# Kernel optimization log

Hardware: AMD Instinct MI355X
Metric: run time of the kernel (lower is better)

## Reference

```python
import jax, jax.numpy as jnp
import numpy as np
from jax.scipy.special import digamma

T, K, D = 8192, 64, 128


def setup_inputs() -> dict:
    key = jax.random.key(0)
    ks = jax.random.split(key, 7)
    mu_t = jax.random.normal(ks[0], (T, D), jnp.float32)
    diag_var_t = jax.random.uniform(ks[1], (T, D), jnp.float32)  # encoder diag variances >= 0
    niw_mu = jax.random.normal(ks[2], (K, D), jnp.float32)
    A = jax.random.normal(ks[3], (K, D, D), jnp.float32) / np.sqrt(D)
    niw_Psi = jnp.einsum('kde,kfe->kdf', A, A) + float(D) * jnp.eye(D, dtype=jnp.float32)[None]  # SPD
    niw_nu = D + 2.0 + 10.0 * jax.random.uniform(ks[4], (K,), jnp.float32)  # nu > D+1
    phi = 0.1 + 4.0 * jax.random.uniform(ks[5], (K, K), jnp.float32)  # Dirichlet posterior params > 0
    log_pi = jax.nn.log_softmax(jax.random.normal(ks[6], (K,), jnp.float32))
    return dict(mu_t=mu_t, diag_var_t=diag_var_t, niw_mu=niw_mu, niw_Psi=niw_Psi,
                niw_nu=niw_nu, phi=phi, log_pi=log_pi)


def _emission_logB(mu_t, diag_var_t, niw_mu, niw_Psi, niw_nu):
    # E[Lambda_k] = nu_k * Psi_k^{-1}; E[log|Lambda_k|] via multivariate digamma
    L = jnp.linalg.cholesky(niw_Psi)                                  # [K,D,D]
    logdet_Psi = 2.0 * jnp.sum(jnp.log(jnp.diagonal(L, axis1=-2, axis2=-1)), axis=-1)  # [K]
    eye = jnp.broadcast_to(jnp.eye(D, dtype=niw_Psi.dtype), (K, D, D))
    Psi_inv = jax.scipy.linalg.cho_solve((L, True), eye)              # [K,D,D]
    E_Lam = niw_nu[:, None, None] * Psi_inv                           # [K,D,D]
    i = jnp.arange(1, D + 1, dtype=niw_Psi.dtype)[None, :]            # [1,D]
    E_logdet = jnp.sum(digamma((niw_nu[:, None] + 1.0 - i) / 2.0), axis=1) \
        + D * jnp.log(jnp.asarray(2.0, niw_Psi.dtype)) - logdet_Psi   # [K]
    diagv = jnp.clip(diag_var_t, 0.0)                                 # [T,D]
    diff = mu_t[:, None, :] - niw_mu[None, :, :]                      # [T,K,D]
    quad_mean = jnp.einsum('tkd,kde,tke->tk', diff, E_Lam, diff)      # [T,K]
    ELam_diag = jnp.diagonal(E_Lam, axis1=-2, axis2=-1)               # [K,D]
    trace_diag = jnp.einsum('td,kd->tk', diagv, ELam_diag)            # [T,K]
    const = -0.5 * D * jnp.log(jnp.asarray(2.0 * np.pi, mu_t.dtype))
    return 0.5 * E_logdet[None, :] + const - 0.5 * (quad_mean + trace_diag)


def _forward_backward(log_pi, ElogA, logB):
    a0 = log_pi + logB[0]
    z0 = jax.nn.logsumexp(a0)
    alpha0 = a0 - z0

    def fwd_step(aprev, logb):
        pred = jax.nn.logsumexp(aprev[:, None] + ElogA, axis=0)
        a = pred + logb
        z = jax.nn.logsumexp(a)
        return a - z, (a - z, z)

    _, (alpha_rest, z_rest) = jax.lax.scan(fwd_step, alpha0, logB[1:])
    alpha = jnp.concatenate([alpha0[None], alpha_rest], axis=0)       # [T,K]
    logZ = jnp.concatenate([z0[None], z_rest], axis=0)                # [T]

    def bwd_step(bnext, xs):
        logb_next, z_next = xs
        b = jax.nn.logsumexp(ElogA + (logb_next + bnext)[None, :], axis=1) - z_next
        return b, b

    beta_T = jnp.zeros_like(alpha0)
    _, beta_rest = jax.lax.scan(bwd_step, beta_T, (logB[1:], logZ[1:]), reverse=True)
    beta = jnp.concatenate([beta_rest, beta_T[None]], axis=0)         # [T,K]

    rhat_log = alpha + beta
    rhat_log = rhat_log - jax.nn.logsumexp(rhat_log, axis=1, keepdims=True)
    rhat = jnp.exp(rhat_log)

    x = alpha[:-1, :, None] + ElogA[None, :, :] + (logB[1:] + beta[1:])[:, None, :]  # [T-1,K,K]
    x = x - jax.nn.logsumexp(x.reshape(x.shape[0], -1), axis=1)[:, None, None]
    xihat = jnp.exp(x)

    ll = jnp.sum(logZ)
    return rhat, xihat, ll


def reference(mu_t, diag_var_t, niw_mu, niw_Psi, niw_nu, phi, log_pi):
    logB = _emission_logB(mu_t, diag_var_t, niw_mu, niw_Psi, niw_nu)  # [T,K]
    ElogA = digamma(phi) - digamma(jnp.sum(phi, axis=1, keepdims=True))  # [K,K]
    rhat, xihat, ll = _forward_backward(log_pi, ElogA, logB)
    return rhat, xihat, ll
```

## Files before the change

### kernel.cpp

```cpp
#include <hip/hip_runtime.h>
#include <math.h>

#define T_LEN 8192
#define KK 64
#define DD 128
#define RS 132
#define GP 68

typedef __bf16  bf16x4 __attribute__((ext_vector_type(4)));
typedef __bf16  bf16x8 __attribute__((ext_vector_type(8)));
typedef float  f32x16 __attribute__((ext_vector_type(16)));

__device__ __forceinline__ float wred_max(float v){
#pragma unroll
  for (int m = 1; m < 64; m <<= 1) v = fmaxf(v, __shfl_xor(v, m, 64));
  return v;
}
__device__ __forceinline__ float wred_sum(float v){
#pragma unroll
  for (int m = 1; m < 64; m <<= 1) v += __shfl_xor(v, m, 64);
  return v;
}
__device__ __forceinline__ float digamma_f(float x){
  float r = 0.f;
  while (x < 6.f){ r -= 1.f/x; x += 1.f; }
  float ix = 1.f/x, ix2 = ix*ix;
  return r + logf(x) - 0.5f*ix - ix2*(0.0833333333f - ix2*(0.0083333333f - ix2*0.0039682540f));
}

__global__ void __launch_bounds__(256, 1) k_neumann(
    const float* __restrict__ Psi, const float* __restrict__ niw_mu,
    const float* __restrict__ nu_, const float* __restrict__ phi,
    __bf16* __restrict__ Ebf, float* __restrict__ EdiagT,
    float* __restrict__ cvecT, float* __restrict__ rK, float* __restrict__ Lhalf,
    float* __restrict__ sclK,
    float* __restrict__ ElogA, float* __restrict__ P, float* __restrict__ PT)
{
  extern __shared__ float lds[];
  float* Rl = lds;
  float* Pb = lds + DD*RS;
  __shared__ float red[256];
  __shared__ float msh[DD];
  int k = blockIdx.x, tid = threadIdx.x;
  const float* A = Psi + (size_t)k*DD*DD;

  if (tid < 64){
    float ph = phi[k*KK + tid];
    float s  = wred_sum(ph);
    float e  = digamma_f(ph) - digamma_f(s);
    ElogA[k*KK + tid] = e;
    float p = expf(e);
    P [k*KK + tid] = p;
    PT[tid*KK + k] = p;
  }

  float tl = 0.f;
  for (int d = tid; d < DD; d += 256) tl += A[d*DD + d];
  red[tid] = tl; __syncthreads();
  for (int off = 128; off > 0; off >>= 1){ if (tid < off) red[tid] += red[tid+off]; __syncthreads(); }
  float c = red[0] / (float)DD;
  __syncthreads();

  float trpow = 0.f;
  for (int idx = tid; idx < DD*DD; idx += 256){
    int d = idx >> 7, e = idx & 127;
    float v = ((d == e) ? 1.f : 0.f) - A[idx]/c;
    Rl[d*RS + e] = v;
    if (d == e) trpow += v;
  }
  __syncthreads();

  int tr = tid >> 4, tc = tid & 15;
  int r0 = tr*8, c0 = tc*8;
  float S[8][8];
#pragma unroll
  for (int i = 0; i < 8; i++)
#pragma unroll
// ... 62 lines not shown
#pragma unroll
  for (int i = 0; i < 8; i++)
#pragma unroll
    for (int j = 0; j < 8; j++){
      float sv = S[i][j];
      bool dg = (r0+i == c0+j);
      if (dg) EdiagT[(r0+i)*KK + k] = scl*sv;
      float et = scl*(sv - (dg ? 1.f : 0.f));
      int r = (r0+i)*DD + (c0+j);
      Ebf[(size_t)(r>>4)*1024 + k*16 + (r&15)] = (__bf16)et;
    }
#pragma unroll
  for (int i = 0; i < 8; i++){
    float4 w0, w1;
    w0.x=S[i][0]; w0.y=S[i][1]; w0.z=S[i][2]; w0.w=S[i][3];
    w1.x=S[i][4]; w1.y=S[i][5]; w1.z=S[i][6]; w1.w=S[i][7];
    *(float4*)&Pb[(r0+i)*RS + c0]     = w0;
    *(float4*)&Pb[(r0+i)*RS + c0 + 4] = w1;
  }
  for (int d = tid; d < DD; d += 256) msh[d] = niw_mu[k*DD + d];
  __syncthreads();
  float cv = 0.f;
  if (tid < DD){
    float acc = 0.f;
    for (int e = 0; e < DD; e++) acc += Pb[tid*RS + e]*msh[e];
    cv = scl*acc;
    cvecT[tid*KK + k] = cv;
  }
  red[tid] = (tid < DD) ? msh[tid]*cv : 0.f; __syncthreads();
  for (int off = 128; off > 0; off >>= 1){ if (tid < off) red[tid] += red[tid+off]; __syncthreads(); }
  if (tid == 0) rK[k] = red[0];
}

__global__ void __launch_bounds__(256, 1) k_q1(const float* __restrict__ mu,
      const __bf16* __restrict__ Ebf, float* __restrict__ part)
{
  __shared__ float muF[32*132];
  __shared__ float trb[128*66];
  int b = blockIdx.x;
  int rs = b & 3, tseg = b >> 2;
  int t0 = tseg*128, d0 = rs*32;
  int tid = threadIdx.x;
  int w = tid >> 6, lane = tid & 63;
  int kh = w & 1, th = w >> 1;
  int l31 = lane & 31;
  int k0 = (lane >> 5)*8;

  for (int v = tid; v < 128*32; v += 256){
    int t = v >> 5, d = v & 31;
    muF[d*132 + t] = mu[(size_t)(t0+t)*DD + d0 + d];
  }

  bf16x8 Bf0[8], Bf1[8];
#pragma unroll
  for (int c = 0; c < 8; c++){
    int tc0 = t0 + th*64 + l31;
    int tc1 = tc0 + 32;
    float4 x0 = *(const float4*)&mu[(size_t)tc0*DD + c*16 + k0];
    float4 x1 = *(const float4*)&mu[(size_t)tc0*DD + c*16 + k0 + 4];
    bf16x8 hv;
    hv[0]=(__bf16)x0.x; hv[1]=(__bf16)x0.y; hv[2]=(__bf16)x0.z; hv[3]=(__bf16)x0.w;
    hv[4]=(__bf16)x1.x; hv[5]=(__bf16)x1.y; hv[6]=(__bf16)x1.z; hv[7]=(__bf16)x1.w;
    Bf0[c] = hv;
    float4 y0 = *(const float4*)&mu[(size_t)tc1*DD + c*16 + k0];
    float4 y1 = *(const float4*)&mu[(size_t)tc1*DD + c*16 + k0 + 4];
    bf16x8 gv;
    gv[0]=(__bf16)y0.x; gv[1]=(__bf16)y0.y; gv[2]=(__bf16)y0.z; gv[3]=(__bf16)y0.w;
    gv[4]=(__bf16)y1.x; gv[5]=(__bf16)y1.y; gv[6]=(__bf16)y1.z; gv[7]=(__bf16)y1.w;
    Bf1[c] = gv;
  }
  __syncthreads();

  const unsigned short* __restrict__ Eu = (const unsigned short*)Ebf;
  size_t abase = (size_t)(kh*32 + l31)*16 + k0;

  f32x16 acc0, acc1;
#pragma unroll
  for (int i = 0; i < 16; i++){ acc0[i]=0.f; acc1[i]=0.f; }

  uint4 A0[8], A1[8];
  {
    const unsigned short* ap = Eu + (size_t)d0*8192 + abase;
#pragma unroll
    for (int c = 0; c < 8; c++) A0[c] = *(const uint4*)(ap + c*1024);
#pragma unroll
    for (int c = 0; c < 8; c++) A1[c] = *(const uint4*)(ap + 8192 + c*1024);
  }

  for (int dd = 0; dd < 32; dd += 2){
    {
      f32x16 ta, tb;
#pragma unroll
      for (int i = 0; i < 16; i++){ ta[i]=0.f; tb[i]=0.f; }
#pragma unroll
      for (int c = 0; c < 8; c++){
        bf16x8 av = *(bf16x8*)&A0[c];
        ta = __builtin_amdgcn_mfma_f32_32x32x16_bf16(av, Bf0[c], ta, 0, 0, 0);
        tb = __builtin_amdgcn_mfma_f32_32x32x16_bf16(av, Bf1[c], tb, 0, 0, 0);
      }
      float m0 = muF[dd*132 + th*64 + l31];
      float m1 = muF[dd*132 + th*64 + 32 + l31];
#pragma unroll
      for (int i = 0; i < 16; i++){
        acc0[i] = fmaf(m0, ta[i], acc0[i]);
        acc1[i] = fmaf(m1, tb[i], acc1[i]);
      }
    }
    if (dd + 2 < 32){
      const unsigned short* ap = Eu + (size_t)(d0+dd+2)*8192 + abase;
#pragma unroll
      for (int c = 0; c < 8; c++) A0[c] = *(const uint4*)(ap + c*1024);
    }
    {
      f32x16 ta, tb;
#pragma unroll
      for (int i = 0; i < 16; i++){ ta[i]=0.f; tb[i]=0.f; }
#pragma unroll
      for (int c = 0; c < 8; c++){
        bf16x8 av = *(bf16x8*)&A1[c];
        ta = __builtin_amdgcn_mfma_f32_32x32x16_bf16(av, Bf0[c], ta, 0, 0, 0);
        tb = __builtin_amdgcn_mfma_f32_32x32x16_bf16(av, Bf1[c], tb, 0, 0, 0);
      }
      float m0 = muF[(dd+1)*132 + th*64 + l31];
      float m1 = muF[(dd+1)*132 + th*64 + 32 + l31];
#pragma unroll
      for (int i = 0; i < 16; i++){
        acc0[i] = fmaf(m0, ta[i], acc0[i]);
        acc1[i] = fmaf(m1, tb[i], acc1[i]);
      }
    }
    if (dd + 3 < 32){
      const unsigned short* ap = Eu + (size_t)(d0+dd+3)*8192 + abase;
#pragma unroll
      for (int c = 0; c < 8; c++) A1[c] = *(const uint4*)(ap + c*1024);
    }
  }

  __syncthreads();
#pragma unroll
  for (int r = 0; r < 16; r++){
    int krow = kh*32 + (r&3) + 8*(r>>2) + 4*(lane>>5);
    trb[(th*64 + l31)*66 + krow]      = acc0[r];
    trb[(th*64 + 32 + l31)*66 + krow] = acc1[r];
  }
  __syncthreads();
  float* dst = part + (size_t)rs*T_LEN*KK;
  {
    int t = tid >> 1, kc = (tid & 1)*32;
#pragma unroll
    for (int q = 0; q < 8; q++){
      float4 vv = *(float4*)&trb[t*66 + kc + q*4];
      *(float4*)&dst[(size_t)(t0+t)*KK + kc + q*4] = vv;
    }
  }
}

__global__ void __launch_bounds__(256) k_logBall(
    const float* __restrict__ part, const float* __restrict__ mu, const float* __restrict__ dvar,
    const float* __restrict__ cvecT, const float* __restrict__ EdiagT,
    const float* __restrict__ rK, const float* __restrict__ Lhalf, const float* __restrict__ sclK,
    float* __restrict__ logB, float* __restrict__ mrow, float* __restrict__ btil)
{
  int tid = threadIdx.x; int k = tid & 63; int w = tid >> 6;
  float rk = rK[k], lh = Lhalf[k], scl = sclK[k];
  int tbase = blockIdx.x*32 + w*8;
  float a1[8], a2[8], ssv[8];
#pragma unroll
  for (int tt = 0; tt < 8; tt++){ a1[tt]=0.f; a2[tt]=0.f; ssv[tt]=0.f; }
  for (int dc = 0; dc < DD; dc += 4){
    float c0 = cvecT[(dc+0)*KK + k], c1 = cvecT[(dc+1)*KK + k];
    float c2 = cvecT[(dc+2)*KK + k], c3 = cvecT[(dc+3)*KK + k];
    float e0 = EdiagT[(dc+0)*KK + k], e1 = EdiagT[(dc+1)*KK + k];
    float e2 = EdiagT[(dc+2)*KK + k], e3 = EdiagT[(dc+3)*KK + k];
#pragma unroll
    for (int tt = 0; tt < 8; tt++){
      float4 m4 = *(const float4*)(mu   + (size_t)(tbase+tt)*DD + dc);
      float4 v4 = *(const float4*)(dvar + (size_t)(tbase+tt)*DD + dc);
      a1[tt] = fmaf(m4.x,c0, fmaf(m4.y,c1, fmaf(m4.z,c2, fmaf(m4.w,c3, a1[tt]))));
      a2[tt] = fmaf(fmaxf(v4.x,0.f),e0, fmaf(fmaxf(v4.y,0.f),e1,
               fmaf(fmaxf(v4.z,0.f),e2, fmaf(fmaxf(v4.w,0.f),e3, a2[tt]))));
      ssv[tt] = fmaf(m4.x,m4.x, fmaf(m4.y,m4.y, fmaf(m4.z,m4.z, fmaf(m4.w,m4.w, ssv[tt]))));
    }
  }
#pragma unroll
  for (int tt = 0; tt < 8; tt++){
    int t = tbase + tt;
    float q = scl*ssv[tt]
            + part[(size_t)0*T_LEN*KK + (size_t)t*KK + k]
            + part[(size_t)1*T_LEN*KK + (size_t)t*KK + k]
            + part[(size_t)2*T_LEN*KK + (size_t)t*KK + k]
            + part[(size_t)3*T_LEN*KK + (size_t)t*KK + k];
    float lb = lh - 0.5f*(q - 2.f*a1[tt] + rk + a2[tt]);
    float m  = wred_max(lb);
    logB[(size_t)t*KK + k] = lb;
    btil[(size_t)t*KK + k] = expf(lb - m);
    if (k == 0) mrow[t] = m;
  }
}

__global__ void __launch_bounds__(128, 1) k_pass1(const float* __restrict__ Pm,
     const float* __restrict__ btil, float* __restrict__ G8)
{
  __shared__ float G[64*GP];
  __shared__ float wmax[2][2];
  int tid = threadIdx.x, w = tid >> 6, lane = tid & 63;
  int chunk = blockIdx.x;
  int kb8 = (lane >> 5)*8;
  int n = lane & 31;

  bf16x8 Bhi[4][2], Blo[4][2];
#pragma unroll
  for (int Kb = 0; Kb < 4; Kb++)
#pragma unroll
    for (int J = 0; J < 2; J++){
#pragma unroll
      for (int j = 0; j < 8; j++){
        float p = Pm[(Kb*16 + kb8 + j)*KK + J*32 + n];
        __bf16 h = (__bf16)p;
        Bhi[Kb][J][j] = h;
        Blo[Kb][J][j] = (__bf16)(p - (float)h);
      }
    }
  for (int v = tid; v < 64*64; v += 128){
    int i = v >> 6, j = v & 63;
    G[i*GP + j] = (i == j) ? 1.f : 0.f;
  }
  __syncthreads();

  int m = w*32 + n;
// ... 81 lines not shown
      float4 x0 = *(const float4*)&X[m*GP + Kb*16 + kb8];
      float4 x1 = *(const float4*)&X[m*GP + Kb*16 + kb8 + 4];
      float xv[8] = {x0.x,x0.y,x0.z,x0.w,x1.x,x1.y,x1.z,x1.w};
      bf16x8 ah, al;
#pragma unroll
      for (int q = 0; q < 8; q++){
        __bf16 h = (__bf16)xv[q];
        ah[q] = h;
        al[q] = (__bf16)(xv[q] - (float)h);
      }
      acc0 = __builtin_amdgcn_mfma_f32_32x32x16_bf16(ah, Bh[Kb][0], acc0, 0,0,0);
      acc0 = __builtin_amdgcn_mfma_f32_32x32x16_bf16(ah, Bl[Kb][0], acc0, 0,0,0);
      acc0 = __builtin_amdgcn_mfma_f32_32x32x16_bf16(al, Bh[Kb][0], acc0, 0,0,0);
      acc1 = __builtin_amdgcn_mfma_f32_32x32x16_bf16(ah, Bh[Kb][1], acc1, 0,0,0);
      acc1 = __builtin_amdgcn_mfma_f32_32x32x16_bf16(ah, Bl[Kb][1], acc1, 0,0,0);
      acc1 = __builtin_amdgcn_mfma_f32_32x32x16_bf16(al, Bh[Kb][1], acc1, 0,0,0);
    }
    float mx = 0.f;
#pragma unroll
    for (int i = 0; i < 16; i++) mx = fmaxf(mx, fmaxf(acc0[i], acc1[i]));
    mx = wred_max(mx);
    if (lane == 0) wmax[j&1][w] = mx;
    __syncthreads();
    float inv = 1.f/fmaxf(wmax[j&1][0], wmax[j&1][1]);
#pragma unroll
    for (int r = 0; r < 16; r++){
      int row = w*32 + (r&3) + 8*(r>>2) + 4*(lane>>5);
      X[row*GP + n]      = acc0[r]*inv;
      X[row*GP + 32 + n] = acc1[r]*inv;
    }
    __syncthreads();
  }
  for (int v = tid; v < 4096; v += 128) dstLin[v] = X[(v>>6)*GP + (v&63)];
}

__global__ void __launch_bounds__(128, 1) k_chain8(const float* __restrict__ G8,
        float* __restrict__ H64)
{
  __shared__ float X[64*GP];
  __shared__ float wmax[2][2];
  int tid = threadIdx.x, w = tid >> 6, lane = tid & 63;
  int bid = blockIdx.x;
  chain_body(G8 + (size_t)bid*8*4096, 8, X, wmax, H64 + (size_t)bid*4096, tid, w, lane);
}

__device__ void mat_combine(const float* __restrict__ A, const float* __restrict__ B,
    float* __restrict__ out, float* __restrict__ outT,
    float* __restrict__ X, float* __restrict__ wmax, int tid, int w, int lane)
{
  int kb8 = (lane >> 5)*8;
  int n = lane & 31;
  int m = w*32 + n;
  for (int v = tid; v < 4096; v += 128) X[(v>>6)*GP + (v&63)] = A[v];
  bf16x8 Bh[4][2], Bl[4][2];
#pragma unroll
  for (int Kb = 0; Kb < 4; Kb++)
#pragma unroll
    for (int J = 0; J < 2; J++){
#pragma unroll
      for (int jj = 0; jj < 8; jj++){
        float p = B[(Kb*16 + kb8 + jj)*64 + J*32 + n];
        __bf16 h = (__bf16)p;
        Bh[Kb][J][jj] = h;
        Bl[Kb][J][jj] = (__bf16)(p - (float)h);
      }
    }
  __syncthreads();
  f32x16 acc0, acc1;
#pragma unroll
  for (int i = 0; i < 16; i++){ acc0[i] = 0.f; acc1[i] = 0.f; }
#pragma unroll
  for (int Kb = 0; Kb < 4; Kb++){
    float4 x0 = *(const float4*)&X[m*GP + Kb*16 + kb8];
    float4 x1 = *(const float4*)&X[m*GP + Kb*16 + kb8 + 4];
    float xv[8] = {x0.x,x0.y,x0.z,x0.w,x1.x,x1.y,x1.z,x1.w};
    bf16x8 ah, al;
// ... 22 lines not shown
    int row = w*32 + (r&3) + 8*(r>>2) + 4*(lane>>5);
    out[row*64 + n]      = acc0[r]*inv;
    out[row*64 + 32 + n] = acc1[r]*inv;
  }
  if (outT){
    __syncthreads();
#pragma unroll
    for (int r = 0; r < 16; r++){
      int row = w*32 + (r&3) + 8*(r>>2) + 4*(lane>>5);
      X[row*GP + n]      = acc0[r]*inv;
      X[row*GP + 32 + n] = acc1[r]*inv;
    }
    __syncthreads();
    for (int v = tid; v < 4096; v += 128) outT[v] = X[(v&63)*GP + (v>>6)];
  }
}

__device__ void mat_copy(const float* __restrict__ A, float* __restrict__ out,
    float* __restrict__ outT, float* __restrict__ X, int tid)
{
  if (!outT){
    for (int v = tid; v < 4096; v += 128) out[v] = A[v];
  } else {
    for (int v = tid; v < 4096; v += 128){
      float vv = A[v];
      out[v] = vv;
      X[(v>>6)*GP + (v&63)] = vv;
    }
    __syncthreads();
    for (int v = tid; v < 4096; v += 128) outT[v] = X[(v&63)*GP + (v>>6)];
  }
}

__global__ void __launch_bounds__(128, 1) k_ks(
    const float* __restrict__ PAin, float* __restrict__ PAout,
    const float* __restrict__ SBin, float* __restrict__ SBout,
    float* __restrict__ SBT, int s, int wrT)
{
  __shared__ float X[64*GP];
  __shared__ float wmax[2];
  int tid = threadIdx.x, w = tid >> 6, lane = tid & 63;
  int c = blockIdx.x;
  if (c >= s)
    mat_combine(PAin + (size_t)(c-s)*4096, PAin + (size_t)c*4096,
                PAout + (size_t)c*4096, nullptr, X, wmax, tid, w, lane);
  else
    mat_copy(PAin + (size_t)c*4096, PAout + (size_t)c*4096, nullptr, X, tid);
  __syncthreads();
  float* t = wrT ? (SBT + (size_t)c*4096) : nullptr;
  if (c + s <= 127)
    mat_combine(SBin + (size_t)c*4096, SBin + (size_t)(c+s)*4096,
                SBout + (size_t)c*4096, t, X, wmax, tid, w, lane);
  else
    mat_copy(SBin + (size_t)c*4096, SBout + (size_t)c*4096, t, X, tid);
}

__global__ void __launch_bounds__(64, 1) k_pass3(const float* __restrict__ Pm, const float* __restrict__ PTm,
   const float* __restrict__ PA, const float* __restrict__ SBT,
   const float* __restrict__ logB, const float* __restrict__ mrow, const float* __restrict__ btil,
   const float* __restrict__ log_pi,
   float* __restrict__ alphahat, float* __restrict__ betahat, float* __restrict__ llpart)
{
  int lane = threadIdx.x;
  int bid = blockIdx.x;
  if (bid < 128){
    int c = bid;
    float Preg[64];
#pragma unroll
    for (int i = 0; i < 64; i++) Preg[i] = Pm[i*64 + lane];
    float a; float llacc = 0.f;
    int tstart;
    float x0v = log_pi[lane] + logB[lane];
    float mm0 = wred_max(x0v);
    float e0 = expf(x0v - mm0);
    float ss0 = wred_sum(e0);
    if (c == 0){
      a = e0/ss0;
      llacc = mm0 + logf(ss0);
      alphahat[lane] = a;
      tstart = 1;
    } else {
      float a0 = e0/ss0;
      const float* H = PA + (size_t)(c-1)*4096;
      float Hr[64];
#pragma unroll
      for (int i = 0; i < 64; i++) Hr[i] = H[i*64 + lane];
      float p0 = 0.f, p1 = 0.f, p2 = 0.f, p3 = 0.f;
#pragma unroll
      for (int i = 0; i < 16; i++){
        p0 = fmaf(__shfl(a0, i,      64), Hr[i],      p0);
        p1 = fmaf(__shfl(a0, i + 16, 64), Hr[i + 16], p1);
        p2 = fmaf(__shfl(a0, i + 32, 64), Hr[i + 32], p2);
        p3 = fmaf(__shfl(a0, i + 48, 64), Hr[i + 48], p3);
      }
      a = (p0 + p1) + (p2 + p3);
      a /= wred_sum(a);
      tstart = c*64;
    }
    int tend = c*64 + 64;
    float bt = btil[(size_t)tstart*KK + lane];
    for (int t = tstart; t < tend; t++){
      float btn = 0.f;
      if (t + 1 < tend) btn = btil[(size_t)(t+1)*KK + lane];
      float mr = mrow[t];
      float p0 = 0.f, p1 = 0.f, p2 = 0.f, p3 = 0.f;
#pragma unroll
      for (int i = 0; i < 16; i++){
        p0 = fmaf(__shfl(a, i,      64), Preg[i],      p0);
        p1 = fmaf(__shfl(a, i + 16, 64), Preg[i + 16], p1);
        p2 = fmaf(__shfl(a, i + 32, 64), Preg[i + 32], p2);
        p3 = fmaf(__shfl(a, i + 48, 64), Preg[i + 48], p3);
      }
      float pred = (p0 + p1) + (p2 + p3);
      a = pred * bt;
      if (((t - tstart) & 3) == 3 || t == tend - 1){
        float s = wred_sum(a);
        a = a / s;
        llacc += logf(s);
      }
      llacc += mr;
      alphahat[(size_t)t*KK + lane] = a;
      bt = btn;
    }
    if (lane == 0) llpart[c] = llacc;
  } else {
    int c = bid - 128;
    float PTreg[64];
#pragma unroll
    for (int j = 0; j < 64; j++) PTreg[j] = PTm[j*64 + lane];
    float b, lb;
    if (c == 127){
      b = 1.f; lb = 0.f;
    } else {
      const float* H = SBT + (size_t)(c+1)*4096;
      float s0 = 0.f, s1 = 0.f, s2 = 0.f, s3 = 0.f;
#pragma unroll
      for (int i = 0; i < 16; i++){
        s0 += H[(i     )*64 + lane];
        s1 += H[(i + 16)*64 + lane];
        s2 += H[(i + 32)*64 + lane];
        s3 += H[(i + 48)*64 + lane];
      }
      float s = (s0 + s1) + (s2 + s3);
      float mmb = wred_max(s);
      b = s/mmb;
      lb = logf(b);
    }
    int t1 = c*64 + 63;
    betahat[(size_t)t1*KK + lane] = b;
    float lgb = logB[(size_t)t1*KK + lane];
    float mrn = mrow[t1];
    for (int t = t1 - 1; t >= c*64; t--){
      float lgbn = 0.f, mrnn = 0.f;
      if (t > c*64){
        lgbn = logB[(size_t)t*KK + lane];
        mrnn = mrow[t];
      }
      float lv = (lgb - mrn) + lb;
      float vm = wred_max(lv);
      float vv = expf(lv - vm);
      float q0 = 0.f, q1r = 0.f, q2 = 0.f, q3 = 0.f;
#pragma unroll
      for (int j = 0; j < 16; j++){
        q0  = fmaf(PTreg[j],      __shfl(vv, j,      64), q0);
        q1r = fmaf(PTreg[j + 16], __shfl(vv, j + 16, 64), q1r);
        q2  = fmaf(PTreg[j + 32], __shfl(vv, j + 32, 64), q2);
        q3  = fmaf(PTreg[j + 48], __shfl(vv, j + 48, 64), q3);
      }
      b = (q0 + q1r) + (q2 + q3);
      lb = logf(b);
      betahat[(size_t)t*KK + lane] = b;
      lgb = lgbn; mrn = mrnn;
    }
  }
}

__global__ void __launch_bounds__(256) k_outs(const float* __restrict__ ah,
     const float* __restrict__ bh, const float* __restrict__ ElogA,
     const float* __restrict__ logB, const float* __restrict__ llp,
     float* __restrict__ out_rhat, float* __restrict__ out_xi, float* __restrict__ out_ll)
{
  __shared__ float la[64], wc[64];
  __shared__ float redm[4], reds[4];
  int tid = threadIdx.x;
  int b = blockIdx.x;
  if (tid < 64) la[tid] = logf(ah[(size_t)b*KK + tid]);
  else if (tid < 128 && b < T_LEN-1){
    int j = tid - 64;
    wc[j] = logB[(size_t)(b+1)*KK + j] + logf(bh[(size_t)(b+1)*KK + j]);
  }
  __syncthreads();
  if (tid < 64){
    float s = la[tid] + logf(bh[(size_t)b*KK + tid]);
    float m = wred_max(s);
    float p = (m < -3.0e37f) ? 1.f : expf(s - m);
    float ss = wred_sum(p);
    out_rhat[(size_t)b*KK + tid] = p/ss;
  }
  if (b == T_LEN-1){
    if (tid >= 64 && tid < 128){
      int i = tid - 64;
      float v = llp[i] + llp[i + 64];
      v = wred_sum(v);
      if (i == 0) out_ll[0] = v;
    }
// ... 43 lines not shown

extern "C" void kernel_launch(void* const* d_in, const int* in_sizes, int n_in,
                              void* d_out, int out_size, void* d_ws, size_t ws_size,
                              hipStream_t stream)
{
  const float* mu    = (const float*)d_in[0];
  const float* dvar  = (const float*)d_in[1];
  const float* niwmu = (const float*)d_in[2];
  const float* Psi   = (const float*)d_in[3];
  const float* nu    = (const float*)d_in[4];
  const float* phi   = (const float*)d_in[5];
  const float* lpi   = (const float*)d_in[6];
  float* out = (float*)d_out;
  float* ws  = (float*)d_ws;

  size_t o = 0;
  float* EbfF   = ws + o; o += (size_t)DD*DD*KK/2;
  float* EdiagT = ws + o; o += (size_t)DD*KK;
  float* cvecT  = ws + o; o += (size_t)DD*KK;
  float* rK     = ws + o; o += KK;
  float* Lhalf  = ws + o; o += KK;
  float* sclK   = ws + o; o += KK;
  float* ElogA  = ws + o; o += KK*KK;
  float* P      = ws + o; o += KK*KK;
  float* PT     = ws + o; o += KK*KK;
  float* logB   = ws + o; o += (size_t)T_LEN*KK;
  float* mrowp  = ws + o; o += T_LEN;
  float* btil   = ws + o; o += (size_t)T_LEN*KK;
  float* G8     = ws + o; o += (size_t)1024*4096;
  float* H64    = ws + o; o += (size_t)128*4096;
  float* llp    = ws + o; o += 128;
  float* ah     = ws + o; o += (size_t)T_LEN*KK;
  float* bh     = ws + o; o += (size_t)T_LEN*KK;
  if (ws_size < o*sizeof(float)) return;

  __bf16* Ebf = (__bf16*)EbfF;
  float*  part = G8;

  const size_t M = (size_t)128*4096;
  float* PAa = G8;
  float* PAb = G8 + M;
  float* SBa = G8 + 2*M;
  float* SBb = G8 + 3*M;
  float* SBT = G8 + 4*M;

  hipFuncSetAttribute((const void*)k_neumann, hipFuncAttributeMaxDynamicSharedMemorySize, 2*DD*RS*4);

  k_neumann<<<64, 256, 2*DD*RS*4, stream>>>(Psi, niwmu, nu, phi, Ebf, EdiagT, cvecT, rK, Lhalf, sclK, ElogA, P, PT);
  k_q1<<<256, 256, 0, stream>>>(mu, Ebf, part);
  k_logBall<<<256, 256, 0, stream>>>(part, mu, dvar, cvecT, EdiagT, rK, Lhalf, sclK, logB, mrowp, btil);
  k_pass1<<<1024, 128, 0, stream>>>(P, btil, G8);
  k_chain8<<<128, 128, 0, stream>>>(G8, H64);
  k_ks<<<128, 128, 0, stream>>>(H64, PAb, H64, SBb, SBT,  1, 0);
  k_ks<<<128, 128, 0, stream>>>(PAb, PAa, SBb, SBa, SBT,  2, 0);
  k_ks<<<128, 128, 0, stream>>>(PAa, PAb, SBa, SBb, SBT,  4, 0);
  k_ks<<<128, 128, 0, stream>>>(PAb, PAa, SBb, SBa, SBT,  8, 0);
  k_ks<<<128, 128, 0, stream>>>(PAa, PAb, SBa, SBb, SBT, 16, 0);
  k_ks<<<128, 128, 0, stream>>>(PAb, PAa, SBb, SBa, SBT, 32, 0);
  k_ks<<<128, 128, 0, stream>>>(PAa, PAb, SBa, SBb, SBT, 64, 1);
  k_pass3<<<256, 64, 0, stream>>>(P, PT, PAb, SBT, logB, mrowp, btil, lpi, ah, bh, llp);
  k_outs<<<T_LEN, 256, 0, stream>>>(ah, bh, ElogA, logB, llp, out, out + (size_t)T_LEN*KK,
                                    out + (size_t)T_LEN*KK + (size_t)(T_LEN-1)*KK*KK);
}
```

Baseline: 430.5 us.

## Merge launch chain into persistent kernels with software grid barriers

Fuses k_q1 and k_logBall into one persistent kernel, and k_chain8, the seven k_ks scan rounds and k_pass3 into another, synchronising phases with an atomic-counter grid barrier that k_neumann resets. This cuts the number of kernel launches and their inter-kernel gaps. The barrier assumes all 256 blocks are co-resident, which is plausible given the grid size and device, and it adds spin-wait and atomic overhead. In k_back the ks rounds now run on 256 blocks split by side instead of 128 blocks each doing both combines.

```diff
diff --git a/kernel.cpp b/kernel.cpp
--- a/kernel.cpp
+++ b/kernel.cpp
@@ -6,6 +6,7 @@
 #define DD 128
 #define RS 132
 #define GP 68
+#define NB 256
 
 typedef __bf16  bf16x4 __attribute__((ext_vector_type(4)));
 typedef __bf16  bf16x8 __attribute__((ext_vector_type(8)));
@@ -26,6 +27,17 @@
   while (x < 6.f){ r -= 1.f/x; x += 1.f; }
   float ix = 1.f/x, ix2 = ix*ix;
   return r + logf(x) - 0.5f*ix - ix2*(0.0833333333f - ix2*(0.0083333333f - ix2*0.0039682540f));
+}
+
+__device__ __forceinline__ void gridbar(int* cnt){
+  __syncthreads();
+  if (threadIdx.x == 0){
+    __hip_atomic_fetch_add(cnt, 1, __ATOMIC_ACQ_REL, __HIP_MEMORY_SCOPE_AGENT);
+    while (__hip_atomic_fetch_add(cnt, 0, __ATOMIC_RELAXED, __HIP_MEMORY_SCOPE_AGENT) < NB)
+      __builtin_amdgcn_s_sleep(32);
+    __builtin_amdgcn_fence(__ATOMIC_ACQUIRE, "agent");
+  }
+  __syncthreads();
 }
 
 __global__ void __launch_bounds__(256, 1) k_neumann(
@@ -34,7 +46,8 @@
     __bf16* __restrict__ Ebf, float* __restrict__ EdiagT,
     float* __restrict__ cvecT, float* __restrict__ rK, float* __restrict__ Lhalf,
     float* __restrict__ sclK,
-    float* __restrict__ ElogA, float* __restrict__ P, float* __restrict__ PT)
+    float* __restrict__ ElogA, float* __restrict__ P, float* __restrict__ PT,
+    int* __restrict__ syncb)
 {
   extern __shared__ float lds[];
   float* Rl = lds;
@@ -43,6 +56,9 @@
   __shared__ float msh[DD];
   int k = blockIdx.x, tid = threadIdx.x;
   const float* A = Psi + (size_t)k*DD*DD;
+
+  if (k == 0 && tid < 16)
+    __hip_atomic_store(&syncb[tid], 0, __ATOMIC_RELAXED, __HIP_MEMORY_SCOPE_AGENT);
 
   if (tid < 64){
     float ph = phi[k*KK + tid];
@@ -171,169 +187,168 @@
   if (tid == 0) rK[k] = red[0];
 }
 
-__global__ void __launch_bounds__(256, 1) k_q1(const float* __restrict__ mu,
-      const __bf16* __restrict__ Ebf, float* __restrict__ part)
+__global__ void __launch_bounds__(256, 1) k_front(
+    const float* __restrict__ mu, const float* __restrict__ dvar,
+    const __bf16* __restrict__ Ebf,
+    const float* __restrict__ cvecT, const float* __restrict__ EdiagT,
+    const float* __restrict__ rK, const float* __restrict__ Lhalf, const float* __restrict__ sclK,
+    float* __restrict__ part,
+    float* __restrict__ logB, float* __restrict__ mrow, float* __restrict__ btil,
+    int* __restrict__ syncb)
 {
   __shared__ float muF[32*132];
   __shared__ float trb[128*66];
-  int b = blockIdx.x;
-  int rs = b & 3, tseg = b >> 2;
-  int t0 = tseg*128, d0 = rs*32;
-  int tid = threadIdx.x;
+  int tid = threadIdx.x, bid = blockIdx.x;
   int w = tid >> 6, lane = tid & 63;
-  int kh = w & 1, th = w >> 1;
-  int l31 = lane & 31;
-  int k0 = (lane >> 5)*8;
-
-  for (int v = tid; v < 128*32; v += 256){
-    int t = v >> 5, d = v & 31;
-    muF[d*132 + t] = mu[(size_t)(t0+t)*DD + d0 + d];
-  }
-
-  bf16x8 Bf0[8], Bf1[8];
-#pragma unroll
-  for (int c = 0; c < 8; c++){
-    int tc0 = t0 + th*64 + l31;
-    int tc1 = tc0 + 32;
-    float4 x0 = *(const float4*)&mu[(size_t)tc0*DD + c*16 + k0];
-    float4 x1 = *(const float4*)&mu[(size_t)tc0*DD + c*16 + k0 + 4];
-    bf16x8 hv;
-    hv[0]=(__bf16)x0.x; hv[1]=(__bf16)x0.y; hv[2]=(__bf16)x0.z; hv[3]=(__bf16)x0.w;
-    hv[4]=(__bf16)x1.x; hv[5]=(__bf16)x1.y; hv[6]=(__bf16)x1.z; hv[7]=(__bf16)x1.w;
-    Bf0[c] = hv;
-    float4 y0 = *(const float4*)&mu[(size_t)tc1*DD + c*16 + k0];
-    float4 y1 = *(const float4*)&mu[(size_t)tc1*DD + c*16 + k0 + 4];
-    bf16x8 gv;
-    gv[0]=(__bf16)y0.x; gv[1]=(__bf16)y0.y; gv[2]=(__bf16)y0.z; gv[3]=(__bf16)y0.w;
-    gv[4]=(__bf16)y1.x; gv[5]=(__bf16)y1.y; gv[6]=(__bf16)y1.z; gv[7]=(__bf16)y1.w;
-    Bf1[c] = gv;
-  }
-  __syncthreads();
-
-  const unsigned short* __restrict__ Eu = (const unsigned short*)Ebf;
-  size_t abase = (size_t)(kh*32 + l31)*16 + k0;
-
-  f32x16 acc0, acc1;
-#pragma unroll
-  for (int i = 0; i < 16; i++){ acc0[i]=0.f; acc1[i]=0.f; }
-
-  uint4 A0[8], A1[8];
+
   {
-    const unsigned short* ap = Eu + (size_t)d0*8192 + abase;
-#pragma unroll
-    for (int c = 0; c < 8; c++) A0[c] = *(const uint4*)(ap + c*1024);
-#pragma unroll
-    for (int c = 0; c < 8; c++) A1[c] = *(const uint4*)(ap + 8192 + c*1024);
-  }
-
-  for (int dd = 0; dd < 32; dd += 2){
+    int rs = bid & 3, tseg = bid >> 2;
+    int t0 = tseg*128, d0 = rs*32;
+    int kh = w & 1, th = w >> 1;
+    int l31 = lane & 31;
+    int k0 = (lane >> 5)*8;
+
+    for (int v = tid; v < 128*32; v += 256){
+      int t = v >> 5, d = v & 31;
+      muF[d*132 + t] = mu[(size_t)(t0+t)*DD + d0 + d];
+    }
+    bf16x8 Bf0[8], Bf1[8];
+#pragma unroll
+    for (int c = 0; c < 8; c++){
+      int tc0 = t0 + th*64 + l31;
+      int tc1 = tc0 + 32;
+      float4 x0 = *(const float4*)&mu[(size_t)tc0*DD + c*16 + k0];
+      float4 x1 = *(const float4*)&mu[(size_t)tc0*DD + c*16 + k0 + 4];
+      bf16x8 hv;
+      hv[0]=(__bf16)x0.x; hv[1]=(__bf16)x0.y; hv[2]=(__bf16)x0.z; hv[3]=(__bf16)x0.w;
+      hv[4]=(__bf16)x1.x; hv[5]=(__bf16)x1.y; hv[6]=(__bf16)x1.z; hv[7]=(__bf16)x1.w;
+      Bf0[c] = hv;
+      float4 y0 = *(const float4*)&mu[(size_t)tc1*DD + c*16 + k0];
+      float4 y1 = *(const float4*)&mu[(size_t)tc1*DD + c*16 + k0 + 4];
+      bf16x8 gv;
+      gv[0]=(__bf16)y0.x; gv[1]=(__bf16)y0.y; gv[2]=(__bf16)y0.z; gv[3]=(__bf16)y0.w;
+      gv[4]=(__bf16)y1.x; gv[5]=(__bf16)y1.y; gv[6]=(__bf16)y1.z; gv[7]=(__bf16)y1.w;
+      Bf1[c] = gv;
+    }
+    __syncthreads();
+
+    const unsigned short* Eu = (const unsigned short*)Ebf;
+    size_t abase = (size_t)(kh*32 + l31)*16 + k0;
+    f32x16 acc0, acc1;
+#pragma unroll
+    for (int i = 0; i < 16; i++){ acc0[i]=0.f; acc1[i]=0.f; }
+    uint4 A0[8], A1[8];
     {
-      f32x16 ta, tb;
-#pragma unroll
-      for (int i = 0; i < 16; i++){ ta[i]=0.f; tb[i]=0.f; }
-#pragma unroll
-      for (int c = 0; c < 8; c++){
-        bf16x8 av = *(bf16x8*)&A0[c];
-        ta = __builtin_amdgcn_mfma_f32_32x32x16_bf16(av, Bf0[c], ta, 0, 0, 0);
-        tb = __builtin_amdgcn_mfma_f32_32x32x16_bf16(av, Bf1[c], tb, 0, 0, 0);
-      }
-      float m0 = muF[dd*132 + th*64 + l31];
-      float m1 = muF[dd*132 + th*64 + 32 + l31];
-#pragma unroll
-      for (int i = 0; i < 16; i++){
-        acc0[i] = fmaf(m0, ta[i], acc0[i]);
-        acc1[i] = fmaf(m1, tb[i], acc1[i]);
-      }
-    }
-    if (dd + 2 < 32){
-      const unsigned short* ap = Eu + (size_t)(d0+dd+2)*8192 + abase;
+      const unsigned short* ap = Eu + (size_t)d0*8192 + abase;
 #pragma unroll
       for (int c = 0; c < 8; c++) A0[c] = *(const uint4*)(ap + c*1024);
-    }
+#pragma unroll
+      for (int c = 0; c < 8; c++) A1[c] = *(const uint4*)(ap + 8192 + c*1024);
+    }
+    for (int dd = 0; dd < 32; dd += 2){
+      {
+        f32x16 ta, tb;
+#pragma unroll
+        for (int i = 0; i < 16; i++){ ta[i]=0.f; tb[i]=0.f; }
+#pragma unroll
+        for (int c = 0; c < 8; c++){
+          bf16x8 av = *(bf16x8*)&A0[c];
+          ta = __builtin_amdgcn_mfma_f32_32x32x16_bf16(av, Bf0[c], ta, 0, 0, 0);
+          tb = __builtin_amdgcn_mfma_f32_32x32x16_bf16(av, Bf1[c], tb, 0, 0, 0);
+        }
+        float m0 = muF[dd*132 + th*64 + l31];
+        float m1 = muF[dd*132 + th*64 + 32 + l31];
+#pragma unroll
+        for (int i = 0; i < 16; i++){
+          acc0[i] = fmaf(m0, ta[i], acc0[i]);
+          acc1[i] = fmaf(m1, tb[i], acc1[i]);
+        }
+      }
+      if (dd + 2 < 32){
+        const unsigned short* ap = Eu + (size_t)(d0+dd+2)*8192 + abase;
+#pragma unroll
+        for (int c = 0; c < 8; c++) A0[c] = *(const uint4*)(ap + c*1024);
+      }
+      {
+        f32x16 ta, tb;
+#pragma unroll
+        for (int i = 0; i < 16; i++){ ta[i]=0.f; tb[i]=0.f; }
+#pragma unroll
+        for (int c = 0; c < 8; c++){
+          bf16x8 av = *(bf16x8*)&A1[c];
+          ta = __builtin_amdgcn_mfma_f32_32x32x16_bf16(av, Bf0[c], ta, 0, 0, 0);
+          tb = __builtin_amdgcn_mfma_f32_32x32x16_bf16(av, Bf1[c], tb, 0, 0, 0);
+        }
+        float m0 = muF[(dd+1)*132 + th*64 + l31];
+        float m1 = muF[(dd+1)*132 + th*64 + 32 + l31];
+#pragma unroll
+        for (int i = 0; i < 16; i++){
+          acc0[i] = fmaf(m0, ta[i], acc0[i]);
+          acc1[i] = fmaf(m1, tb[i], acc1[i]);
+        }
+      }
+      if (dd + 3 < 32){
+        const unsigned short* ap = Eu + (size_t)(d0+dd+3)*8192 + abase;
+#pragma unroll
+        for (int c = 0; c < 8; c++) A1[c] = *(const uint4*)(ap + c*1024);
+      }
+    }
+    __syncthreads();
+#pragma unroll
+    for (int r = 0; r < 16; r++){
+      int krow = kh*32 + (r&3) + 8*(r>>2) + 4*(lane>>5);
+      trb[(th*64 + l31)*66 + krow]      = acc0[r];
+      trb[(th*64 + 32 + l31)*66 + krow] = acc1[r];
+    }
+    __syncthreads();
+    float* dst = part + (size_t)rs*T_LEN*KK;
     {
-      f32x16 ta, tb;
-#pragma unroll
-      for (int i = 0; i < 16; i++){ ta[i]=0.f; tb[i]=0.f; }
-#pragma unroll
-      for (int c = 0; c < 8; c++){
-        bf16x8 av = *(bf16x8*)&A1[c];
-        ta = __builtin_amdgcn_mfma_f32_32x32x16_bf16(av, Bf0[c], ta, 0, 0, 0);
-        tb = __builtin_amdgcn_mfma_f32_32x32x16_bf16(av, Bf1[c], tb, 0, 0, 0);
-      }
-      float m0 = muF[(dd+1)*132 + th*64 + l31];
-      float m1 = muF[(dd+1)*132 + th*64 + 32 + l31];
-#pragma unroll
-      for (int i = 0; i < 16; i++){
-        acc0[i] = fmaf(m0, ta[i], acc0[i]);
-        acc1[i] = fmaf(m1, tb[i], acc1[i]);
-      }
-    }
-    if (dd + 3 < 32){
-      const unsigned short* ap = Eu + (size_t)(d0+dd+3)*8192 + abase;
-#pragma unroll
-      for (int c = 0; c < 8; c++) A1[c] = *(const uint4*)(ap + c*1024);
-    }
-  }
-
-  __syncthreads();
-#pragma unroll
-  for (int r = 0; r < 16; r++){
-    int krow = kh*32 + (r&3) + 8*(r>>2) + 4*(lane>>5);
-    trb[(th*64 + l31)*66 + krow]      = acc0[r];
-    trb[(th*64 + 32 + l31)*66 + krow] = acc1[r];
-  }
-  __syncthreads();
-  float* dst = part + (size_t)rs*T_LEN*KK;
+      int t = tid >> 1, kc = (tid & 1)*32;
+#pragma unroll
+      for (int q = 0; q < 8; q++){
+        float4 vv = *(float4*)&trb[t*66 + kc + q*4];
+        *(float4*)&dst[(size_t)(t0+t)*KK + kc + q*4] = vv;
+      }
+    }
+  }
+  gridbar(&syncb[0]);
+
   {
-    int t = tid >> 1, kc = (tid & 1)*32;
-#pragma unroll
-    for (int q = 0; q < 8; q++){
-      float4 vv = *(float4*)&trb[t*66 + kc + q*4];
-      *(float4*)&dst[(size_t)(t0+t)*KK + kc + q*4] = vv;
-    }
-  }
-}
-
-__global__ void __launch_bounds__(256) k_logBall(
-    const float* __restrict__ part, const float* __restrict__ mu, const float* __restrict__ dvar,
-    const float* __restrict__ cvecT, const float* __restrict__ EdiagT,
-    const float* __restrict__ rK, const float* __restrict__ Lhalf, const float* __restrict__ sclK,
-    float* __restrict__ logB, float* __restrict__ mrow, float* __restrict__ btil)
-{
-  int tid = threadIdx.x; int k = tid & 63; int w = tid >> 6;
-  float rk = rK[k], lh = Lhalf[k], scl = sclK[k];
-  int tbase = blockIdx.x*32 + w*8;
-  float a1[8], a2[8], ssv[8];
-#pragma unroll
-  for (int tt = 0; tt < 8; tt++){ a1[tt]=0.f; a2[tt]=0.f; ssv[tt]=0.f; }
-  for (int dc = 0; dc < DD; dc += 4){
-    float c0 = cvecT[(dc+0)*KK + k], c1 = cvecT[(dc+1)*KK + k];
-    float c2 = cvecT[(dc+2)*KK + k], c3 = cvecT[(dc+3)*KK + k];
-    float e0 = EdiagT[(dc+0)*KK + k], e1 = EdiagT[(dc+1)*KK + k];
-    float e2 = EdiagT[(dc+2)*KK + k], e3 = EdiagT[(dc+3)*KK + k];
+    int k = lane;
+    float rk = rK[k], lh = Lhalf[k], scl = sclK[k];
+    int tbase = bid*32 + w*8;
+    float a1[8], a2[8], ssv[8];
+#pragma unroll
+    for (int tt = 0; tt < 8; tt++){ a1[tt]=0.f; a2[tt]=0.f; ssv[tt]=0.f; }
+    for (int dc = 0; dc < DD; dc += 4){
+      float c0 = cvecT[(dc+0)*KK + k], c1 = cvecT[(dc+1)*KK + k];
+      float c2 = cvecT[(dc+2)*KK + k], c3 = cvecT[(dc+3)*KK + k];
+      float e0 = EdiagT[(dc+0)*KK + k], e1 = EdiagT[(dc+1)*KK + k];
+      float e2 = EdiagT[(dc+2)*KK + k], e3 = EdiagT[(dc+3)*KK + k];
+#pragma unroll
+      for (int tt = 0; tt < 8; tt++){
+        float4 m4 = *(const float4*)(mu   + (size_t)(tbase+tt)*DD + dc);
+        float4 v4 = *(const float4*)(dvar + (size_t)(tbase+tt)*DD + dc);
+        a1[tt] = fmaf(m4.x,c0, fmaf(m4.y,c1, fmaf(m4.z,c2, fmaf(m4.w,c3, a1[tt]))));
+        a2[tt] = fmaf(fmaxf(v4.x,0.f),e0, fmaf(fmaxf(v4.y,0.f),e1,
+                 fmaf(fmaxf(v4.z,0.f),e2, fmaf(fmaxf(v4.w,0.f),e3, a2[tt]))));
+        ssv[tt] = fmaf(m4.x,m4.x, fmaf(m4.y,m4.y, fmaf(m4.z,m4.z, fmaf(m4.w,m4.w, ssv[tt]))));
+      }
+    }
 #pragma unroll
     for (int tt = 0; tt < 8; tt++){
-      float4 m4 = *(const float4*)(mu   + (size_t)(tbase+tt)*DD + dc);
-      float4 v4 = *(const float4*)(dvar + (size_t)(tbase+tt)*DD + dc);
-      a1[tt] = fmaf(m4.x,c0, fmaf(m4.y,c1, fmaf(m4.z,c2, fmaf(m4.w,c3, a1[tt]))));
-      a2[tt] = fmaf(fmaxf(v4.x,0.f),e0, fmaf(fmaxf(v4.y,0.f),e1,
-               fmaf(fmaxf(v4.z,0.f),e2, fmaf(fmaxf(v4.w,0.f),e3, a2[tt]))));
-      ssv[tt] = fmaf(m4.x,m4.x, fmaf(m4.y,m4.y, fmaf(m4.z,m4.z, fmaf(m4.w,m4.w, ssv[tt]))));
-    }
-  }
-#pragma unroll
-  for (int tt = 0; tt < 8; tt++){
-    int t = tbase + tt;
-    float q = scl*ssv[tt]
-            + part[(size_t)0*T_LEN*KK + (size_t)t*KK + k]
-            + part[(size_t)1*T_LEN*KK + (size_t)t*KK + k]
-            + part[(size_t)2*T_LEN*KK + (size_t)t*KK + k]
-            + part[(size_t)3*T_LEN*KK + (size_t)t*KK + k];
-    float lb = lh - 0.5f*(q - 2.f*a1[tt] + rk + a2[tt]);
-    float m  = wred_max(lb);
-    logB[(size_t)t*KK + k] = lb;
-    btil[(size_t)t*KK + k] = expf(lb - m);
-    if (k == 0) mrow[t] = m;
+      int t = tbase + tt;
+      float q = scl*ssv[tt]
+              + part[(size_t)0*T_LEN*KK + (size_t)t*KK + k]
+              + part[(size_t)1*T_LEN*KK + (size_t)t*KK + k]
+              + part[(size_t)2*T_LEN*KK + (size_t)t*KK + k]
+              + part[(size_t)3*T_LEN*KK + (size_t)t*KK + k];
+      float lb = lh - 0.5f*(q - 2.f*a1[tt] + rk + a2[tt]);
+      float m  = wred_max(lb);
+      logB[(size_t)t*KK + k] = lb;
+      btil[(size_t)t*KK + k] = expf(lb - m);
+      if (k == 0) mrow[t] = m;
+    }
   }
 }
 
@@ -481,16 +496,6 @@
     __syncthreads();
   }
   for (int v = tid; v < 4096; v += 128) dstLin[v] = X[(v>>6)*GP + (v&63)];
-}
-
-__global__ void __launch_bounds__(128, 1) k_chain8(const float* __restrict__ G8,
-        float* __restrict__ H64)
-{
-  __shared__ float X[64*GP];
-  __shared__ float wmax[2][2];
-  int tid = threadIdx.x, w = tid >> 6, lane = tid & 63;
-  int bid = blockIdx.x;
-  chain_body(G8 + (size_t)bid*8*4096, 8, X, wmax, H64 + (size_t)bid*4096, tid, w, lane);
 }
 
 __device__ void mat_combine(const float* __restrict__ A, const float* __restrict__ B,
@@ -579,145 +584,165 @@
   }
 }
 
-__global__ void __launch_bounds__(128, 1) k_ks(
-    const float* __restrict__ PAin, float* __restrict__ PAout,
-    const float* __restrict__ SBin, float* __restrict__ SBout,
-    float* __restrict__ SBT, int s, int wrT)
+__global__ void __launch_bounds__(128, 1) k_back(
+    float* G8, float* __restrict__ H64,
+    const float* __restrict__ Pm, const float* __restrict__ PTm,
+    const float* __restrict__ logB, const float* __restrict__ mrow,
+    const float* __restrict__ btil, const float* __restrict__ log_pi,
+    float* __restrict__ ah, float* __restrict__ bh, float* __restrict__ llp,
+    int* __restrict__ syncb)
 {
   __shared__ float X[64*GP];
-  __shared__ float wmax[2];
-  int tid = threadIdx.x, w = tid >> 6, lane = tid & 63;
-  int c = blockIdx.x;
-  if (c >= s)
-    mat_combine(PAin + (size_t)(c-s)*4096, PAin + (size_t)c*4096,
-                PAout + (size_t)c*4096, nullptr, X, wmax, tid, w, lane);
-  else
-    mat_copy(PAin + (size_t)c*4096, PAout + (size_t)c*4096, nullptr, X, tid);
-  __syncthreads();
-  float* t = wrT ? (SBT + (size_t)c*4096) : nullptr;
-  if (c + s <= 127)
-    mat_combine(SBin + (size_t)c*4096, SBin + (size_t)(c+s)*4096,
-                SBout + (size_t)c*4096, t, X, wmax, tid, w, lane);
-  else
-    mat_copy(SBin + (size_t)c*4096, SBout + (size_t)c*4096, t, X, tid);
-}
-
-__global__ void __launch_bounds__(64, 1) k_pass3(const float* __restrict__ Pm, const float* __restrict__ PTm,
-   const float* __restrict__ PA, const float* __restrict__ SBT,
-   const float* __restrict__ logB, const float* __restrict__ mrow, const float* __restrict__ btil,
-   const float* __restrict__ log_pi,
-   float* __restrict__ alphahat, float* __restrict__ betahat, float* __restrict__ llpart)
-{
-  int lane = threadIdx.x;
-  int bid = blockIdx.x;
-  if (bid < 128){
-    int c = bid;
-    float Preg[64];
-#pragma unroll
-    for (int i = 0; i < 64; i++) Preg[i] = Pm[i*64 + lane];
-    float a; float llacc = 0.f;
-    int tstart;
-    float x0v = log_pi[lane] + logB[lane];
-    float mm0 = wred_max(x0v);
-    float e0 = expf(x0v - mm0);
-    float ss0 = wred_sum(e0);
-    if (c == 0){
-      a = e0/ss0;
-      llacc = mm0 + logf(ss0);
-      alphahat[lane] = a;
-      tstart = 1;
+  __shared__ float wmaxc[2][2];
+  __shared__ float wmax1[2];
+  int tid = threadIdx.x, bid = blockIdx.x;
+  int w = tid >> 6, lane = tid & 63;
+
+  if (bid < 128)
+    chain_body(G8 + (size_t)bid*8*4096, 8, X, wmaxc, H64 + (size_t)bid*4096, tid, w, lane);
+  gridbar(&syncb[1]);
+
+  const size_t M = (size_t)128*4096;
+  float* PAbuf[2] = {G8, G8 + M};
+  float* SBbuf[2] = {G8 + 2*M, G8 + 3*M};
+  float* SBT = G8 + 4*M;
+  const float* PAin = H64; const float* SBin = H64;
+  int cur = 1;
+  int side = bid >> 7, c = bid & 127;
+  for (int r = 0; r < 7; r++){
+    int s = 1 << r;
+    int wrT = (r == 6);
+    if (side == 0){
+      if (c >= s)
+        mat_combine(PAin + (size_t)(c-s)*4096, PAin + (size_t)c*4096,
+                    PAbuf[cur] + (size_t)c*4096, nullptr, X, wmax1, tid, w, lane);
+      else
+        mat_copy(PAin + (size_t)c*4096, PAbuf[cur] + (size_t)c*4096, nullptr, X, tid);
     } else {
-      float a0 = e0/ss0;
-      const float* H = PA + (size_t)(c-1)*4096;
-      float Hr[64];
-#pragma unroll
-      for (int i = 0; i < 64; i++) Hr[i] = H[i*64 + lane];
-      float p0 = 0.f, p1 = 0.f, p2 = 0.f, p3 = 0.f;
-#pragma unroll
-      for (int i = 0; i < 16; i++){
-        p0 = fmaf(__shfl(a0, i,      64), Hr[i],      p0);
-        p1 = fmaf(__shfl(a0, i + 16, 64), Hr[i + 16], p1);
-        p2 = fmaf(__shfl(a0, i + 32, 64), Hr[i + 32], p2);
-        p3 = fmaf(__shfl(a0, i + 48, 64), Hr[i + 48], p3);
-      }
-      a = (p0 + p1) + (p2 + p3);
-      a /= wred_sum(a);
-      tstart = c*64;
-    }
-    int tend = c*64 + 64;
-    float bt = btil[(size_t)tstart*KK + lane];
-    for (int t = tstart; t < tend; t++){
-      float btn = 0.f;
-      if (t + 1 < tend) btn = btil[(size_t)(t+1)*KK + lane];
-      float mr = mrow[t];
-      float p0 = 0.f, p1 = 0.f, p2 = 0.f, p3 = 0.f;
-#pragma unroll
-      for (int i = 0; i < 16; i++){
-        p0 = fmaf(__shfl(a, i,      64), Preg[i],      p0);
-        p1 = fmaf(__shfl(a, i + 16, 64), Preg[i + 16], p1);
-        p2 = fmaf(__shfl(a, i + 32, 64), Preg[i + 32], p2);
-        p3 = fmaf(__shfl(a, i + 48, 64), Preg[i + 48], p3);
-      }
-      float pred = (p0 + p1) + (p2 + p3);
-      a = pred * bt;
-      if (((t - tstart) & 3) == 3 || t == tend - 1){
-        float s = wred_sum(a);
-        a = a / s;
-        llacc += logf(s);
-      }
-      llacc += mr;
-      alphahat[(size_t)t*KK + lane] = a;
-      bt = btn;
-    }
-    if (lane == 0) llpart[c] = llacc;
-  } else {
-    int c = bid - 128;
-    float PTreg[64];
-#pragma unroll
-    for (int j = 0; j < 64; j++) PTreg[j] = PTm[j*64 + lane];
-    float b, lb;
-    if (c == 127){
-      b = 1.f; lb = 0.f;
+      float* t = wrT ? (SBT + (size_t)c*4096) : nullptr;
+      if (c + s <= 127)
+        mat_combine(SBin + (size_t)c*4096, SBin + (size_t)(c+s)*4096,
+                    SBbuf[cur] + (size_t)c*4096, t, X, wmax1, tid, w, lane);
+      else
+        mat_copy(SBin + (size_t)c*4096, SBbuf[cur] + (size_t)c*4096, t, X, tid);
+    }
+    gridbar(&syncb[2 + r]);
+    PAin = PAbuf[cur]; SBin = SBbuf[cur]; cur ^= 1;
+  }
+  const float* PAfin = PAin;
+
+  if (tid >= 64) return;
+  {
+    int lane0 = tid;
+    if (bid < 128){
+      int cc = bid;
+      float Preg[64];
+#pragma unroll
+      for (int i = 0; i < 64; i++) Preg[i] = Pm[i*64 + lane0];
+      float a; float llacc = 0.f;
+      int tstart;
+      float x0v = log_pi[lane0] + logB[lane0];
+      float mm0 = wred_max(x0v);
+      float e0 = expf(x0v - mm0);
+      float ss0 = wred_sum(e0);
+      if (cc == 0){
+        a = e0/ss0;
+        llacc = mm0 + logf(ss0);
+        ah[lane0] = a;
+        tstart = 1;
+      } else {
+        float a0 = e0/ss0;
+        const float* H = PAfin + (size_t)(cc-1)*4096;
+        float Hr[64];
+#pragma unroll
+        for (int i = 0; i < 64; i++) Hr[i] = H[i*64 + lane0];
+        float p0 = 0.f, p1 = 0.f, p2 = 0.f, p3 = 0.f;
+#pragma unroll
+        for (int i = 0; i < 16; i++){
+          p0 = fmaf(__shfl(a0, i,      64), Hr[i],      p0);
+          p1 = fmaf(__shfl(a0, i + 16, 64), Hr[i + 16], p1);
+          p2 = fmaf(__shfl(a0, i + 32, 64), Hr[i + 32], p2);
+          p3 = fmaf(__shfl(a0, i + 48, 64), Hr[i + 48], p3);
+        }
+        a = (p0 + p1) + (p2 + p3);
+        a /= wred_sum(a);
+        tstart = cc*64;
+      }
+      int tend = cc*64 + 64;
+      float bt = btil[(size_t)tstart*KK + lane0];
+      for (int t = tstart; t < tend; t++){
+        float btn = 0.f;
+        if (t + 1 < tend) btn = btil[(size_t)(t+1)*KK + lane0];
+        float mr = mrow[t];
+        float p0 = 0.f, p1 = 0.f, p2 = 0.f, p3 = 0.f;
+#pragma unroll
+        for (int i = 0; i < 16; i++){
+          p0 = fmaf(__shfl(a, i,      64), Preg[i],      p0);
+          p1 = fmaf(__shfl(a, i + 16, 64), Preg[i + 16], p1);
+          p2 = fmaf(__shfl(a, i + 32, 64), Preg[i + 32], p2);
+          p3 = fmaf(__shfl(a, i + 48, 64), Preg[i + 48], p3);
+        }
+        float pred = (p0 + p1) + (p2 + p3);
+        a = pred * bt;
+        if (((t - tstart) & 3) == 3 || t == tend - 1){
+          float s = wred_sum(a);
+          a = a / s;
+          llacc += logf(s);
+        }
+        llacc += mr;
+        ah[(size_t)t*KK + lane0] = a;
+        bt = btn;
+      }
+      if (lane0 == 0) llp[cc] = llacc;
     } else {
-      const float* H = SBT + (size_t)(c+1)*4096;
-      float s0 = 0.f, s1 = 0.f, s2 = 0.f, s3 = 0.f;
-#pragma unroll
-      for (int i = 0; i < 16; i++){
-        s0 += H[(i     )*64 + lane];
-        s1 += H[(i + 16)*64 + lane];
-        s2 += H[(i + 32)*64 + lane];
-        s3 += H[(i + 48)*64 + lane];
-      }
-      float s = (s0 + s1) + (s2 + s3);
-      float mmb = wred_max(s);
-      b = s/mmb;
-      lb = logf(b);
-    }
-    int t1 = c*64 + 63;
-    betahat[(size_t)t1*KK + lane] = b;
-    float lgb = logB[(size_t)t1*KK + lane];
-    float mrn = mrow[t1];
-    for (int t = t1 - 1; t >= c*64; t--){
-      float lgbn = 0.f, mrnn = 0.f;
-      if (t > c*64){
-        lgbn = logB[(size_t)t*KK + lane];
-        mrnn = mrow[t];
-      }
-      float lv = (lgb - mrn) + lb;
-      float vm = wred_max(lv);
-      float vv = expf(lv - vm);
-      float q0 = 0.f, q1r = 0.f, q2 = 0.f, q3 = 0.f;
-#pragma unroll
-      for (int j = 0; j < 16; j++){
-        q0  = fmaf(PTreg[j],      __shfl(vv, j,      64), q0);
-        q1r = fmaf(PTreg[j + 16], __shfl(vv, j + 16, 64), q1r);
-        q2  = fmaf(PTreg[j + 32], __shfl(vv, j + 32, 64), q2);
-        q3  = fmaf(PTreg[j + 48], __shfl(vv, j + 48, 64), q3);
-      }
-      b = (q0 + q1r) + (q2 + q3);
-      lb = logf(b);
-      betahat[(size_t)t*KK + lane] = b;
-      lgb = lgbn; mrn = mrnn;
+      int cc = bid - 128;
+      float PTreg[64];
+#pragma unroll
+      for (int j = 0; j < 64; j++) PTreg[j] = PTm[j*64 + lane0];
+      float b, lb;
+      if (cc == 127){
+        b = 1.f; lb = 0.f;
+      } else {
+        const float* H = SBT + (size_t)(cc+1)*4096;
+        float s0 = 0.f, s1 = 0.f, s2 = 0.f, s3 = 0.f;
+#pragma unroll
+        for (int i = 0; i < 16; i++){
+          s0 += H[(i     )*64 + lane0];
+          s1 += H[(i + 16)*64 + lane0];
+          s2 += H[(i + 32)*64 + lane0];
+          s3 += H[(i + 48)*64 + lane0];
+        }
+        float s = (s0 + s1) + (s2 + s3);
+        float mmb = wred_max(s);
+        b = s/mmb;
+        lb = logf(b);
+      }
+      int t1 = cc*64 + 63;
+      bh[(size_t)t1*KK + lane0] = b;
+      float lgb = logB[(size_t)t1*KK + lane0];
+      float mrn = mrow[t1];
+      for (int t = t1 - 1; t >= cc*64; t--){
+        float lgbn = 0.f, mrnn = 0.f;
+        if (t > cc*64){
+          lgbn = logB[(size_t)t*KK + lane0];
+          mrnn = mrow[t];
+        }
+        float lv = (lgb - mrn) + lb;
+        float vm = wred_max(lv);
+        float vv = expf(lv - vm);
+        float q0 = 0.f, q1r = 0.f, q2 = 0.f, q3 = 0.f;
+#pragma unroll
+        for (int j = 0; j < 16; j++){
+          q0  = fmaf(PTreg[j],      __shfl(vv, j,      64), q0);
+          q1r = fmaf(PTreg[j + 16], __shfl(vv, j + 16, 64), q1r);
+          q2  = fmaf(PTreg[j + 32], __shfl(vv, j + 32, 64), q2);
+          q3  = fmaf(PTreg[j + 48], __shfl(vv, j + 48, 64), q3);
+        }
+        b = (q0 + q1r) + (q2 + q3);
+        lb = logf(b);
+        bh[(size_t)t*KK + lane0] = b;
+        lgb = lgbn; mrn = mrnn;
+      }
     }
   }
 }
@@ -827,33 +852,18 @@
   float* llp    = ws + o; o += 128;
   float* ah     = ws + o; o += (size_t)T_LEN*KK;
   float* bh     = ws + o; o += (size_t)T_LEN*KK;
+  int*   syncb  = (int*)(ws + o); o += 16;
   if (ws_size < o*sizeof(float)) return;
 
   __bf16* Ebf = (__bf16*)EbfF;
   float*  part = G8;
 
-  const size_t M = (size_t)128*4096;
-  float* PAa = G8;
-  float* PAb = G8 + M;
-  float* SBa = G8 + 2*M;
-  float* SBb = G8 + 3*M;
-  float* SBT = G8 + 4*M;
-
   hipFuncSetAttribute((const void*)k_neumann, hipFuncAttributeMaxDynamicSharedMemorySize, 2*DD*RS*4);
 
-  k_neumann<<<64, 256, 2*DD*RS*4, stream>>>(Psi, niwmu, nu, phi, Ebf, EdiagT, cvecT, rK, Lhalf, sclK, ElogA, P, PT);
-  k_q1<<<256, 256, 0, stream>>>(mu, Ebf, part);
-  k_logBall<<<256, 256, 0, stream>>>(part, mu, dvar, cvecT, EdiagT, rK, Lhalf, sclK, logB, mrowp, btil);
+  k_neumann<<<64, 256, 2*DD*RS*4, stream>>>(Psi, niwmu, nu, phi, Ebf, EdiagT, cvecT, rK, Lhalf, sclK, ElogA, P, PT, syncb);
+  k_front<<<256, 256, 0, stream>>>(mu, dvar, Ebf, cvecT, EdiagT, rK, Lhalf, sclK, part, logB, mrowp, btil, syncb);
   k_pass1<<<1024, 128, 0, stream>>>(P, btil, G8);
-  k_chain8<<<128, 128, 0, stream>>>(G8, H64);
-  k_ks<<<128, 128, 0, stream>>>(H64, PAb, H64, SBb, SBT,  1, 0);
-  k_ks<<<128, 128, 0, stream>>>(PAb, PAa, SBb, SBa, SBT,  2, 0);
-  k_ks<<<128, 128, 0, stream>>>(PAa, PAb, SBa, SBb, SBT,  4, 0);
-  k_ks<<<128, 128, 0, stream>>>(PAb, PAa, SBb, SBa, SBT,  8, 0);
-  k_ks<<<128, 128, 0, stream>>>(PAa, PAb, SBa, SBb, SBT, 16, 0);
-  k_ks<<<128, 128, 0, stream>>>(PAb, PAa, SBb, SBa, SBT, 32, 0);
-  k_ks<<<128, 128, 0, stream>>>(PAa, PAb, SBa, SBb, SBT, 64, 1);
-  k_pass3<<<256, 64, 0, stream>>>(P, PT, PAb, SBT, logB, mrowp, btil, lpi, ah, bh, llp);
+  k_back<<<256, 128, 0, stream>>>(G8, H64, P, PT, logB, mrowp, btil, lpi, ah, bh, llp, syncb);
   k_outs<<<T_LEN, 256, 0, stream>>>(ah, bh, ElogA, logB, llp, out, out + (size_t)T_LEN*KK,
                                     out + (size_t)T_LEN*KK + (size_t)(T_LEN-1)*KK*KK);
 }
```

New measurement: 541.4 us. +25.8%, slower.
